# Performance work log

Hardware: AMD Instinct MI355X
Metric: run time of the kernel (lower is better)

The kernel has to match this reference:

```python
import jax, jax.numpy as jnp
import numpy as np
from itertools import product

SPATIAL1 = (41, 1600, 1408)  # (z,y,x) = grid[::-1] + [1,0,0]
NUM_BATCH = 2
BN_EPS = 1e-3

# ---------- numpy rulebook construction (spconv-style, done once on host) ----------

def _encode(c, shape):
    D, H, W = [int(v) for v in shape]
    return ((c[:, 0].astype(np.int64) * D + c[:, 1]) * H + c[:, 2]) * W + c[:, 3]

def _lookup(skeys, order, cand):
    pos = np.clip(np.searchsorted(skeys, cand), 0, len(skeys) - 1)
    hit = skeys[pos] == cand
    return hit, order[pos]

def _pad_rb(pairs, n_in, n_out):
    P = max(max(len(a) for a, _ in pairs), 1)
    K = len(pairs)
    ii = np.full((K, P), n_in, np.int32)   # sentinel -> zero feature row
    oo = np.full((K, P), n_out, np.int32)  # sentinel -> dummy output row
    for k, (a, b) in enumerate(pairs):
        ii[k, :len(a)] = a
        oo[k, :len(b)] = b
    return ii, oo

def _subm_rb(coords, shape):
    # SubMConv3d k=3 p=1 s=1: output sites == input sites
    N = len(coords)
    keys = _encode(coords, shape)
    order = np.argsort(keys); skeys = keys[order]
    dims = np.array(shape)
    pairs = []
    for off in product((-1, 0, 1), repeat=3):
        nb = coords[:, 1:] + np.array(off)
        ok = (nb >= 0).all(1) & (nb < dims).all(1)
        oid = np.nonzero(ok)[0]
        cand = _encode(np.concatenate([coords[ok, :1], nb[ok]], 1), shape)
        hit, iid = _lookup(skeys, order, cand)
        pairs.append((iid[hit].astype(np.int32), oid[hit].astype(np.int32)))
    return _pad_rb(pairs, N, N)

def _down_rb(coords, in_shape, ks, st, pd):
    # SparseConv3d: output site active iff any kernel tap hits an active input
    dims = np.array(in_shape); ks = np.array(ks); st = np.array(st); pd = np.array(pd)
    out_shape = (dims + 2 * pd - ks) // st + 1
    offs = list(product(*[range(int(k)) for k in ks]))
    outs = []
    for off in offs:
        o = coords[:, 1:] + pd - np.array(off)
        ok = (o % st == 0).all(1)
        od = o // st
        ok &= (od >= 0).all(1) & (od < out_shape).all(1)
        outs.append(np.concatenate([coords[ok, :1], od[ok]], 1))
    out_coords = np.unique(np.concatenate(outs, 0), axis=0)
    keys = _encode(coords, in_shape)
    order = np.argsort(keys); skeys = keys[order]
    pairs = []
    for off in offs:
        ic = out_coords[:, 1:] * st - pd + np.array(off)
        ok = (ic >= 0).all(1) & (ic < dims).all(1)
        oid = np.nonzero(ok)[0]
        cand = _encode(np.concatenate([out_coords[ok, :1], ic[ok]], 1), in_shape)
        hit, iid = _lookup(skeys, order, cand)
        pairs.append((iid[hit].astype(np.int32), oid[hit].astype(np.int32)))
    ii, oo = _pad_rb(pairs, len(coords), len(out_coords))
    return ii, oo, out_coords, tuple(int(v) for v in out_shape)

def _gen_coords(rng):
    # clustered LiDAR-like active voxels (surfaces -> local density)
    D, H, W = SPATIAL1
    per = []
    for b in range(NUM_BATCH):
        centers = rng.integers([3, 30, 30], [D - 4, H - 31, W - 31], size=(600, 3))
        pts = centers[:, None, :] + rng.integers(-3, 4, size=(600, 60, 3))
        pts = np.clip(pts.reshape(-1, 3), 0, np.array([D - 1, H - 1, W - 1]))
        uniq = np.unique(pts, axis=0)
        per.append(np.concatenate([np.full((len(uniq), 1), b, np.int64), uniq], 1))
    return np.concatenate(per, 0)

CHANS = [(27, 4, 16), (27, 16, 16), (27, 16, 32), (27, 32, 32), (27, 32, 32),
         (27, 32, 64), (27, 64, 64), (27, 64, 64), (27, 64, 64), (27, 64, 64),
         (27, 64, 64), (3, 64, 128)]

def setup_inputs() -> dict:
    rng = np.random.default_rng(0)
    coords = _gen_coords(rng)  # (N,4) [b,z,y,x]
    N = len(coords)
    s1i, s1o = _subm_rb(coords, SPATIAL1)
    d2i, d2o, c2, s2 = _down_rb(coords, SPATIAL1, (3, 3, 3), (2, 2, 2), (1, 1, 1))
    s2i, s2o = _subm_rb(c2, s2)
    d3i, d3o, c3, s3 = _down_rb(c2, s2, (3, 3, 3), (2, 2, 2), (1, 1, 1))
    s3i, s3o = _subm_rb(c3, s3)
    d4i, d4o, c4, s4 = _down_rb(c3, s3, (3, 3, 3), (2, 2, 2), (0, 1, 1))
    s4i, s4o = _subm_rb(c4, s4)
    oi, oo, c5, s5 = _down_rb(c4, s4, (3, 1, 1), (2, 1, 1), (0, 0, 0))

    key = jax.random.key(0)
    ks = jax.random.split(key, 40)
    inp = {}
    for i, (K, ci, co) in enumerate(CHANS):
        inp[f"w{i}"] = (jax.random.normal(ks[i], (K, ci, co), jnp.float32)
                         / np.sqrt(K * ci)).astype(jnp.float32)
        kb = jax.random.split(ks[12 + i], 4)
        inp[f"bn{i}"] = jnp.stack([
            jax.random.uniform(kb[0], (co,)) + 0.5,   # gamma
            jax.random.normal(kb[1], (co,)) * 0.1,    # beta
            jax.random.normal(kb[2], (co,)) * 0.1,    # running mean
            jax.random.uniform(kb[3], (co,)) + 0.5,   # running var
        ]).astype(jnp.float32)
    inp["voxels"] = jax.random.normal(ks[30], (N, 5, 4), jnp.float32)
    inp["voxel_num_points"] = jax.random.randint(ks[31], (N,), 0, 6).astype(jnp.int32)
    for name, arr in [("subm1_in", s1i), ("subm1_out", s1o), ("down2_in", d2i),
                      ("down2_out", d2o), ("subm2_in", s2i), ("subm2_out", s2o),
                      ("down3_in", d3i), ("down3_out", d3o), ("subm3_in", s3i),
                      ("subm3_out", s3o), ("down4_in", d4i), ("down4_out", d4o),
                      ("subm4_in", s4i), ("subm4_out", s4o), ("out_in", oi),
                      ("out_out", oo)]:
        inp[name] = jnp.asarray(arr)
    inp["batch_idx"] = jnp.asarray(c5[:, 0].astype(np.int32))
    inp["n2"] = len(c2); inp["n3"] = len(c3); inp["n4"] = len(c4); inp["n5"] = len(c5)
    inp["n_batch"] = NUM_BATCH
    return inp

# ---------- jax forward ----------

def _sconv(feats, w, in_idx, out_idx, n_out):
    # gather -> per-kernel-offset GEMM -> scatter-add (spconv implicit GEMM)
    fpad = jnp.concatenate([feats, jnp.zeros((1, feats.shape[1]), feats.dtype)], 0)
    g = fpad[in_idx]                                  # (K,P,Cin)
    contrib = jnp.einsum('kpi,kio->kpo', g, w)        # (K,P,Cout)
    out = jnp.zeros((n_out + 1, w.shape[2]), feats.dtype)
    return out.at[out_idx].add(contrib)[:n_out]

def _bnrelu(x, bn):
    g, b, m, v = bn  # eval-mode BatchNorm1d, eps=1e-3
    return jax.nn.relu((x - m) * jax.lax.rsqrt(v + BN_EPS) * g + b)

def reference(voxels, voxel_num_points, w0, w1, w2, w3, w4, w5, w6, w7, w8, w9,
              w10, w11, bn0, bn1, bn2, bn3, bn4, bn5, bn6, bn7, bn8, bn9, bn10,
              bn11, subm1_in, subm1_out, down2_in, down2_out, subm2_in, subm2_out,
              down3_in, down3_out, subm3_in, subm3_out, down4_in, down4_out,
              subm4_in, subm4_out, out_in, out_out, batch_idx, n2, n3, n4, n5,
              n_batch):
    # mean-VFE: average point features per voxel
    denom = jnp.maximum(voxel_num_points.astype(voxels.dtype), 1.0)[:, None]
    x = voxels.sum(1) / denom                              # (N,4)
    n1 = x.shape[0]
    x = _bnrelu(_sconv(x, w0, subm1_in, subm1_out, n1), bn0)   # conv_input
    x = _bnrelu(_sconv(x, w1, subm1_in, subm1_out, n1), bn1)   # conv1
    x = _bnrelu(_sconv(x, w2, down2_in, down2_out, n2), bn2)   # conv2 (s2)
    x = _bnrelu(_sconv(x, w3, subm2_in, subm2_out, n2), bn3)
    x = _bnrelu(_sconv(x, w4, subm2_in, subm2_out, n2), bn4)
    x = _bnrelu(_sconv(x, w5, down3_in, down3_out, n3), bn5)   # conv3 (s2)
    x = _bnrelu(_sconv(x, w6, subm3_in, subm3_out, n3), bn6)
    x = _bnrelu(_sconv(x, w7, subm3_in, subm3_out, n3), bn7)
    x = _bnrelu(_sconv(x, w8, down4_in, down4_out, n4), bn8)   # conv4 (s2)
    x = _bnrelu(_sconv(x, w9, subm4_in, subm4_out, n4), bn9)
    x = _bnrelu(_sconv(x, w10, subm4_in, subm4_out, n4), bn10)
    x = _bnrelu(_sconv(x, w11, out_in, out_out, n5), bn11)     # conv_out
    # dc_feats: per-sample global max pool over active voxels (== max_pool1d)
    dc = jax.ops.segment_max(x, batch_idx, num_segments=n_batch)
    return dc
```

## Files before the change

### kernel.cpp

```cpp
#include <hip/hip_runtime.h>

#define TPB 256
typedef unsigned short u16;
typedef __attribute__((ext_vector_type(8))) short short8v;
typedef __attribute__((ext_vector_type(4))) float f32x4;

__device__ __forceinline__ u16 f2bf(float x) {
    unsigned u = __float_as_uint(x);
    return (u16)((u + 0x7FFFu + ((u >> 16) & 1u)) >> 16);
}
__device__ __forceinline__ float bf2f(u16 h) {
    return __uint_as_float(((unsigned)h) << 16);
}

template<int CS>
__device__ __forceinline__ int swzc(int r, int c) {
    constexpr int PH = (CS == 8) ? 0 : 1;
    return c ^ ((r >> PH) & (CS - 1));
}

__device__ __forceinline__ int xcd_swz(int bid, int nwg) {
    int q = nwg >> 3, r = nwg & 7;
    int x = bid & 7, idx = bid >> 3;
    return (x < r ? x * (q + 1) : r * (q + 1) + (x - r) * q) + idx;
}

__device__ __forceinline__ void gld16(const u16* g, u16* l) {
    __builtin_amdgcn_global_load_lds(
        (const __attribute__((address_space(1))) void*)g,
        (__attribute__((address_space(3))) void*)l, 16, 0, 0);
}

__global__ void vfe_kernel(const float* __restrict__ voxels,
                           const int* __restrict__ nump,
                           float* __restrict__ x, int N) {
    int i = blockIdx.x * blockDim.x + threadIdx.x;
    if (i >= N * 4) return;
    int n = i >> 2, c = i & 3;
    const float* v = voxels + (long)n * 20 + c;
    float s = v[0] + v[4] + v[8] + v[12] + v[16];
    x[i] = s / fmaxf((float)nump[n], 1.0f);
}

struct IBE { const int* rin; const int* rout; int* inv; int P, K, n_in, n_out, KP; };
struct IBA { IBE e[8]; };
__global__ void inv_build_all_kernel(IBA a, long grand) {
    long t = (long)blockIdx.x * blockDim.x + threadIdx.x;
    if (t >= grand) return;
    #pragma unroll
    for (int i = 0; i < 8; ++i) {
        if (t < a.e[i].KP) {
            const IBE& E = a.e[i];
            int ii = E.rin[t];
            if (ii != E.n_in) {
                int k = (int)(t / E.P);
                E.inv[(long)k * E.n_out + E.rout[t]] = ii;
            }
            return;
        }
        t -= a.e[i].KP;
    }
}

struct WPE { const float* w; u16* oh; u16* ol; int K, ci, co, total, paired; };
struct WPA { WPE e[11]; };
__global__ void wprep_kernel(WPA a, long grand) {
    long t = (long)blockIdx.x * blockDim.x + threadIdx.x;
    if (t >= grand) return;
    #pragma unroll
    for (int i = 0; i < 11; ++i) {
        if (t < a.e[i].total) {
            const WPE& E = a.e[i];
            if (E.paired) {
                int p = (int)(t / (E.co * 32));
                int rem = (int)(t % (E.co * 32));
                int o = rem / 32, ci = rem % 32;
                int tap = 2 * p + (ci >> 4);
                float x = (tap < 27) ? E.w[((long)tap * 16 + (ci & 15)) * E.co + o] : 0.f;
                u16 h = f2bf(x);
                float lf = x - bf2f(h);
                int ch = ci >> 3, e = ci & 7;
                int sch = ch ^ ((o >> 1) & 3);
                long d = ((long)p * E.co + o) * 32 + sch * 8 + e;
                E.oh[d] = h; E.ol[d] = f2bf(lf);
            } else {
                int cc = E.ci * E.co;
                int k = (int)(t / cc), r = (int)(t % cc), c = r / E.co, o = r % E.co;
                float x = E.w[t];
                u16 h = f2bf(x);
                float lf = x - bf2f(h);
                int cs = E.ci >> 3, ph = (cs == 8) ? 0 : 1;
                int ch = c >> 3, e = c & 7;
                int sch = ch ^ ((o >> ph) & (cs - 1));
                long d = ((long)k * E.co + o) * E.ci + sch * 8 + e;
                E.oh[d] = h; E.ol[d] = f2bf(lf);
            }
            return;
        }
        t -= a.e[i].total;
    }
}

template<int CO, int K>
__global__ __launch_bounds__(256)
void dconv4_kernel(const float* __restrict__ feats,
                   const float* __restrict__ w,
                   const float* __restrict__ bn,
                   const int* __restrict__ inv, int inv_n,
                   u16* __restrict__ oh, u16* __restrict__ ol,
                   int n_out) {
    constexpr int OG = CO / 4;
    __shared__ float sW[K * 4 * CO];
    for (int i = threadIdx.x; i < K * 4 * CO; i += 256) sW[i] = w[i];
    __syncthreads();
    long t = (long)blockIdx.x * 256 + threadIdx.x;
    int row = (int)(t / OG), og = (int)(t % OG);
    if (row >= n_out) return;
    float a0 = 0.f, a1 = 0.f, a2 = 0.f, a3 = 0.f;
    for (int k = 0; k < K; ++k) {
        int idx = inv[(long)k * inv_n + row];
        if (idx < 0) continue;
        float4 av = *(const float4*)(feats + (long)idx * 4);
        const float* wk = sW + k * 4 * CO + og * 4;
        #pragma unroll
        for (int ci = 0; ci < 4; ++ci) {
            float a = (&av.x)[ci];
            a0 = fmaf(a, wk[ci * CO + 0], a0);
            a1 = fmaf(a, wk[ci * CO + 1], a1);
            a2 = fmaf(a, wk[ci * CO + 2], a2);
            a3 = fmaf(a, wk[ci * CO + 3], a3);
        }
    }
    float4 g = *(const float4*)(bn + og * 4);
    float4 b = *(const float4*)(bn + CO + og * 4);
    float4 m = *(const float4*)(bn + 2 * CO + og * 4);
    float4 v = *(const float4*)(bn + 3 * CO + og * 4);
    float o4[4];
    o4[0] = fmaxf((a0 - m.x) * rsqrtf(v.x + 1e-3f) * g.x + b.x, 0.f);
    o4[1] = fmaxf((a1 - m.y) * rsqrtf(v.y + 1e-3f) * g.y + b.y, 0.f);
    o4[2] = fmaxf((a2 - m.z) * rsqrtf(v.z + 1e-3f) * g.z + b.z, 0.f);
    o4[3] = fmaxf((a3 - m.w) * rsqrtf(v.w + 1e-3f) * g.w + b.w, 0.f);
    long base = (long)row * CO + og * 4;
    #pragma unroll
    for (int c = 0; c < 4; ++c) {
        u16 h = f2bf(o4[c]);
        oh[base + c] = h;
        ol[base + c] = f2bf(o4[c] - bf2f(h));
    }
}

template<int CI, int CO, int KPt, int KT, bool PAIRED, int EPI>
__global__ __launch_bounds__(256, 4)
void mconv_kernel(const u16* __restrict__ fh, const u16* __restrict__ fl,
                  const u16* __restrict__ wh, const u16* __restrict__ wl,
                  const int* __restrict__ inv,
                  const u16* __restrict__ zpage,
                  float* __restrict__ part, long slab_elems,
                  const float* __restrict__ bn,
                  u16* __restrict__ oh, u16* __restrict__ ol,
                  float* __restrict__ outf,
                  int n_out, int kpb) {
    constexpr int CS  = CI / 8;
    constexpr int LCS = (CS == 8) ? 3 : 2;
    constexpr int PH  = (CS == 8) ? 0 : 1;
    constexpr int KS  = CI / 32;
    constexpr int WC  = (CO >= 32) ? 2 : 1;
    constexpr int MT  = (WC == 2) ? 2 : 1;
    constexpr int NTW = CO / (16 * WC);
    constexpr int ASL = 64 * CS;
    constexpr int BSL = CO * CS;
    constexpr int AIT = (ASL + 255) / 256;
    constexpr int BIT = (BSL + 255) / 256;

    __shared__ __align__(16) u16 sAh[64 * CI];
    __shared__ __align__(16) u16 sAl[64 * CI];
    __shared__ __align__(16) u16 sBh[CO * CI];
    __shared__ __align__(16) u16 sBl[CO * CI];

    const int t = threadIdx.x;
    const int bx = xcd_swz(blockIdx.x, gridDim.x);
    const int brow = bx * 64;
    const int kbeg = blockIdx.y * kpb;
    const int kend = (kbeg + kpb < KPt) ? (kbeg + kpb) : KPt;

    const int lane = t & 63, wid = t >> 6;
    const int wr = wid / WC, wc = wid % WC;
    const int frow = lane & 15;
    const int fch  = lane >> 4;

    f32x4 acc[MT][NTW];
    #pragma unroll
    for (int mt = 0; mt < MT; ++mt)
        #pragma unroll
        for (int nt = 0; nt < NTW; ++nt) {
            acc[mt][nt][0] = 0.f; acc[mt][nt][1] = 0.f;
            acc[mt][nt][2] = 0.f; acc[mt][nt][3] = 0.f;
        }

    auto stage = [&](int k) {
        #pragma unroll
        for (int s = 0; s < AIT; ++s) {
            int slot = s * 256 + t;
            if (ASL % 256 == 0 || slot < ASL) {
                int r = slot >> LCS, cc = slot & (CS - 1);
                int c = cc ^ ((r >> PH) & (CS - 1));
                int grow = brow + r;
                const u16 *srcH, *srcL;
                if (PAIRED) {
                    int tap = 2 * k + (c >> 1);
                    int idx = (grow < n_out && tap < KT)
                              ? inv[(long)tap * n_out + grow] : -1;
                    srcH = (idx >= 0) ? fh + (long)idx * 16 + (c & 1) * 8 : zpage;
                    srcL = (idx >= 0) ? fl + (long)idx * 16 + (c & 1) * 8 : zpage;
                } else {
                    int idx = (grow < n_out) ? inv[(long)k * n_out + grow] : -1;
                    srcH = (idx >= 0) ? fh + (long)idx * CI + c * 8 : zpage;
                    srcL = (idx >= 0) ? fl + (long)idx * CI + c * 8 : zpage;
                }
                gld16(srcH, sAh + (s * 256 + wid * 64) * 8);
                gld16(srcL, sAl + (s * 256 + wid * 64) * 8);
            }
        }
        const u16* gbh = wh + (long)k * CO * CI;
        const u16* gbl = wl + (long)k * CO * CI;
        #pragma unroll
        for (int s = 0; s < BIT; ++s) {
            int slot = s * 256 + t;
            if (BSL % 256 == 0 || slot < BSL) {
                gld16(gbh + (long)slot * 8, sBh + (s * 256 + wid * 64) * 8);
                gld16(gbl + (long)slot * 8, sBl + (s * 256 + wid * 64) * 8);
            }
        }
    };
    auto compute = [&]() {
        #pragma unroll
        for (int ks = 0; ks < KS; ++ks) {
            int c = ks * 4 + fch;
            short8v ah[MT], al[MT];
            #pragma unroll
            for (int mt = 0; mt < MT; ++mt) {
                int r = wr * (MT * 16) + mt * 16 + frow;
                int o = r * CI + swzc<CS>(r, c) * 8;
                ah[mt] = *(const short8v*)(sAh + o);
                al[mt] = *(const short8v*)(sAl + o);
            }
            #pragma unroll
            for (int nt = 0; nt < NTW; ++nt) {
                int col = wc * (CO / WC) + nt * 16 + frow;
                int o = col * CI + swzc<CS>(col, c) * 8;
                short8v bh = *(const short8v*)(sBh + o);
                short8v bl = *(const short8v*)(sBl + o);
                #pragma unroll
                for (int mt = 0; mt < MT; ++mt) {
                    acc[mt][nt] = __builtin_amdgcn_mfma_f32_16x16x32_bf16(ah[mt], bh, acc[mt][nt], 0, 0, 0);
                    acc[mt][nt] = __builtin_amdgcn_mfma_f32_16x16x32_bf16(ah[mt], bl, acc[mt][nt], 0, 0, 0);
                    acc[mt][nt] = __builtin_amdgcn_mfma_f32_16x16x32_bf16(al[mt], bh, acc[mt][nt], 0, 0, 0);
                }
            }
        }
    };

    for (int k = kbeg; k < kend; ++k) {
        stage(k);
        __syncthreads();
        compute();
        if (k + 1 < kend) __syncthreads();
    }

    if constexpr (EPI == 0) {
        float* dst = part + (long)blockIdx.y * slab_elems;
        #pragma unroll
        for (int mt = 0; mt < MT; ++mt) {
            int orow0 = brow + wr * (MT * 16) + mt * 16 + (lane >> 4) * 4;
            #pragma unroll
            for (int nt = 0; nt < NTW; ++nt) {
                int ocol = wc * (CO / WC) + nt * 16 + (lane & 15);
                #pragma unroll
                for (int j = 0; j < 4; ++j) {
                    int r = orow0 + j;
                    if (r < n_out) dst[(long)r * CO + ocol] = acc[mt][nt][j];
                }
            }
        }
    } else {
        #pragma unroll
        for (int mt = 0; mt < MT; ++mt) {
            int orow0 = brow + wr * (MT * 16) + mt * 16 + (lane >> 4) * 4;
            #pragma unroll
            for (int nt = 0; nt < NTW; ++nt) {
                int ocol = wc * (CO / WC) + nt * 16 + (lane & 15);
                float g = bn[ocol], bb = bn[CO + ocol];
                float m = bn[2 * CO + ocol], vv = bn[3 * CO + ocol];
                float sc = rsqrtf(vv + 1e-3f) * g;
                #pragma unroll
                for (int j = 0; j < 4; ++j) {
                    int r = orow0 + j;
                    if (r < n_out) {
                        float yv = fmaxf((acc[mt][nt][j] - m) * sc + bb, 0.f);
                        if constexpr (EPI == 1) {
                            u16 h = f2bf(yv);
                            oh[(long)r * CO + ocol] = h;
                            ol[(long)r * CO + ocol] = f2bf(yv - bf2f(h));
                        } else {
                            outf[(long)r * CO + ocol] = yv;
                        }
                    }
                }
            }
        }
    }
}

template<bool EMIT16>
__global__ void reduce_bnrelu_kernel(const float* __restrict__ part, long stride,
                                     int ys, const float* __restrict__ bn, int co,
                                     float* __restrict__ outf,
                                     u16* __restrict__ oh, u16* __restrict__ ol,
                                     long total) {
    long t = (long)blockIdx.x * blockDim.x + threadIdx.x;
    if (t >= total) return;
    float s = 0.f;
    for (int y = 0; y < ys; ++y) s += part[(long)y * stride + t];
    int o = (int)(t % co);
    float g = bn[o], b = bn[co + o], m = bn[2 * co + o], v = bn[3 * co + o];
    float yv = fmaxf((s - m) * rsqrtf(v + 1e-3f) * g + b, 0.f);
    if (EMIT16) {
        u16 h = f2bf(yv);
        oh[t] = h;
        ol[t] = f2bf(yv - bf2f(h));
    } else {
        outf[t] = yv;
    }
}

__global__ void segmax_kernel(const float* __restrict__ x,
                              const int* __restrict__ bidx,
                              float* __restrict__ out, int rows, int nb) {
    __shared__ float sM[8 * 128];
    for (int i = threadIdx.x; i < nb * 128; i += 256) sM[i] = 0.f;
    __syncthreads();
    int c = threadIdx.x & 127;
    int sub = threadIdx.x >> 7;
    for (int r = blockIdx.x * 2 + sub; r < rows; r += gridDim.x * 2) {
        float v = x[(long)r * 128 + c];
        int b = bidx[r];
        atomicMax((int*)&sM[b * 128 + c], __float_as_int(v));
    }
    __syncthreads();
    for (int i = threadIdx.x; i < nb * 128; i += 256)
        atomicMax((int*)out + i, __float_as_int(sM[i]));
}

extern "C" void kernel_launch(void* const* d_in, const int* in_sizes, int n_in,
                              void* d_out, int out_size, void* d_ws, size_t ws_size,
                              hipStream_t stream) {
    (void)n_in;
    const float* voxels = (const float*)d_in[24];
    const int*   nump   = (const int*)d_in[25];
    const int N  = in_sizes[25];
    const int n2 = in_sizes[30] / 27;
    const int n3 = in_sizes[34] / 27;
    const int n4 = in_sizes[38] / 27;
    const int n5 = in_sizes[42];

    struct L { int wi, rb, K, ci, co, nin, nout; };
    const L layers[12] = {
        {0,  26, 27,  4,  16, N,  N }, {1,  26, 27, 16,  16, N,  N },
        {2,  28, 27, 16,  32, N,  n2}, {3,  30, 27, 32,  32, n2, n2},
        {4,  30, 27, 32,  32, n2, n2}, {5,  32, 27, 32,  64, n2, n3},
        {6,  34, 27, 64,  64, n3, n3}, {7,  34, 27, 64,  64, n3, n3},
        {8,  36, 27, 64,  64, n3, n4}, {9,  38, 27, 64,  64, n4, n4},
        {10, 38, 27, 64,  64, n4, n4}, {11, 40,  3, 64, 128, n4, n5},
    };
    struct RBD { int rb, K, nin, nout; };
    const RBD rbs[8] = {
        {26, 27, N,  N }, {28, 27, N,  n2}, {30, 27, n2, n2}, {32, 27, n2, n3},
        {34, 27, n3, n3}, {36, 27, n3, n4}, {38, 27, n4, n4}, {40, 3,  n4, n5},
    };
    const int invmap[12] = {0, 0, 1, 2, 2, 3, 4, 4, 5, 6, 6, 7};

    size_t feat_elems = (size_t)N * 4, wt_elems = 0, arena_elems = 0;
    for (int i = 0; i < 12; ++i) {
        size_t fe = (size_t)layers[i].nout * layers[i].co;
        if (fe > feat_elems) feat_elems = fe;
        if (i >= 3) wt_elems += (size_t)layers[i].K * layers[i].ci * layers[i].co;
    }
    for (int r = 0; r < 8; ++r) arena_elems += (size_t)rbs[r].nout * rbs[r].K;
    const size_t wp1_elems = 14 * 32 * 16;
    const size_t wp2_elems = 14 * 32 * 32;
    auto al = [](size_t x) { return (x + 255) & ~(size_t)255; };
    char* p = (char*)d_ws;
    u16*   zpage = (u16*)p; p += 256;
    int*   inv_arena = (int*)p; p += al(arena_elems * 4);
    float* bufA = (float*)p; p += al(feat_elems * 4);
    u16* ph[2]; u16* pl[2];
    ph[0] = (u16*)p; p += al(feat_elems * 2);
    pl[0] = (u16*)p; p += al(feat_elems * 2);
    ph[1] = (u16*)p; p += al(feat_elems * 2);
    pl[1] = (u16*)p; p += al(feat_elems * 2);
    u16* wth = (u16*)p; p += al(wt_elems * 2);
    u16* wtl = (u16*)p; p += al(wt_elems * 2);
    u16* wp1h = (u16*)p; p += al(wp1_elems * 2);
    u16* wp1l = (u16*)p; p += al(wp1_elems * 2);
    u16* wp2h = (u16*)p; p += al(wp2_elems * 2);
    u16* wp2l = (u16*)p; p += al(wp2_elems * 2);
    float* slab = (float*)p;
    size_t slab_budget = ws_size - (size_t)((char*)slab - (char*)d_ws);

    hipMemsetAsync(zpage, 0, 256, stream);

    int* invs[8];
    {
        size_t off = 0;
        for (int r = 0; r < 8; ++r) { invs[r] = inv_arena + off; off += (size_t)rbs[r].nout * rbs[r].K; }
        hipMemsetAsync(inv_arena, 0xFF, arena_elems * sizeof(int), stream);
        IBA ia;
        long grand = 0;
        for (int r = 0; r < 8; ++r) {
            int P  = in_sizes[rbs[r].rb] / rbs[r].K;
            ia.e[r].rin  = (const int*)d_in[rbs[r].rb];
            ia.e[r].rout = (const int*)d_in[rbs[r].rb + 1];
            ia.e[r].inv  = invs[r];
            ia.e[r].P = P; ia.e[r].K = rbs[r].K; ia.e[r].n_in = rbs[r].nin;
            ia.e[r].n_out = rbs[r].nout;
            ia.e[r].KP = rbs[r].K * P;
            grand += ia.e[r].KP;
        }
        inv_build_all_kernel<<<dim3((unsigned)((grand + TPB - 1) / TPB)), dim3(TPB), 0, stream>>>(ia, grand);
    }

    {
        long tot = (long)N * 4;
        vfe_kernel<<<dim3((unsigned)((tot + TPB - 1) / TPB)), dim3(TPB), 0, stream>>>(
            voxels, nump, bufA, N);
    }

    size_t woff[9];
    {
        WPA wa;
        size_t off = 0;
        for (int i = 0; i < 9; ++i) {
            const L& l = layers[i + 3];
            woff[i] = off;
            wa.e[i].w  = (const float*)d_in[2 * l.wi];
            wa.e[i].oh = wth + off;
            wa.e[i].ol = wtl + off;
            wa.e[i].K = l.K; wa.e[i].ci = l.ci; wa.e[i].co = l.co;
            wa.e[i].total = l.K * l.ci * l.co;
            wa.e[i].paired = 0;
            off += (size_t)wa.e[i].total;
        }
        wa.e[9]  = { (const float*)d_in[2], wp1h, wp1l, 27, 16, 16, (int)wp1_elems, 1 };
        wa.e[10] = { (const float*)d_in[4], wp2h, wp2l, 27, 16, 32, (int)wp2_elems, 1 };
        long grand = (long)off + wp1_elems + wp2_elems;
        wprep_kernel<<<dim3((unsigned)((grand + TPB - 1) / TPB)), dim3(TPB), 0, stream>>>(wa, grand);
    }

    {
        const L& l = layers[0];
        long tot = (long)l.nout * 4;
        dconv4_kernel<16, 27><<<dim3((unsigned)((tot + 255) / 256)), 256, 0, stream>>>(
            bufA, (const float*)d_in[0], (const float*)d_in[1], invs[0], l.nout,
            ph[0], pl[0], l.nout);
    }

    int cset = 0;
    for (int i = 1; i < 12; ++i) {
        const L& l = layers[i];
        const int* invp = invs[invmap[i]];
        unsigned blocks = (unsigned)((l.nout + 63) / 64);
        int KPv = (i <= 2) ? 14 : l.K;
        int ysmax = (KPv == 14) ? 9 : ((KPv == 27) ? 27 : 3);
        size_t per = (size_t)l.nout * l.co * 4;
        int ys = 1;
        while (ys < ysmax && blocks * (unsigned)ys < 768) ys *= 3;
        if (ys > ysmax) ys = ysmax;
        while (ys > 1 && (size_t)ys * per > slab_budget) ys /= 3;
        int kpb = (KPv + ys - 1) / ys;
        long slab_elems = (long)l.nout * l.co;
        dim3 grid(blocks, (unsigned)ys);
        const float* bn = (const float*)d_in[2 * l.wi + 1];
        const u16* fh = ph[cset];
        const u16* fl = pl[cset];
        const u16* whp = (i >= 3) ? wth + woff[i - 3] : nullptr;
        const u16* wlp = (i >= 3) ? wtl + woff[i - 3] : nullptr;

        #define MCONV(CI_, CO_, KP_, KT_, PRD_, WH_, WL_)                              \
            do {                                                                       \
                if (ys == 1 && i < 11)                                                 \
                    mconv_kernel<CI_, CO_, KP_, KT_, PRD_, 1><<<grid, 256, 0, stream>>>( \
                        fh, fl, WH_, WL_, invp, zpage, nullptr, 0, bn,                 \
                        ph[cset ^ 1], pl[cset ^ 1], nullptr, l.nout, kpb);             \
                else if (ys == 1)                                                      \
                    mconv_kernel<CI_, CO_, KP_, KT_, PRD_, 2><<<grid, 256, 0, stream>>>( \
                        fh, fl, WH_, WL_, invp, zpage, nullptr, 0, bn,                 \
                        nullptr, nullptr, bufA, l.nout, kpb);                          \
                else                                                                   \
                    mconv_kernel<CI_, CO_, KP_, KT_, PRD_, 0><<<grid, 256, 0, stream>>>( \
                        fh, fl, WH_, WL_, invp, zpage, slab, slab_elems, bn,           \
                        nullptr, nullptr, nullptr, l.nout, kpb);                       \
            } while (0)

        switch (i) {
        case 1:          MCONV(32, 16, 14, 27, true,  wp1h, wp1l); break;
        case 2:          MCONV(32, 32, 14, 27, true,  wp2h, wp2l); break;
        case 3: case 4:  MCONV(32, 32, 27, 27, false, whp, wlp);   break;
        case 5:          MCONV(32, 64, 27, 27, false, whp, wlp);   break;
        case 11:         MCONV(64, 128, 3, 3,  false, whp, wlp);   break;
        default:         MCONV(64, 64, 27, 27, false, whp, wlp);   break;
        }
        #undef MCONV

        if (ys == 1) {
            if (i < 11) cset ^= 1;
        } else {
            long total = (long)l.nout * l.co;
            unsigned rblocks = (unsigned)((total + TPB - 1) / TPB);
            if (i < 11) {
                reduce_bnrelu_kernel<true><<<dim3(rblocks), dim3(TPB), 0, stream>>>(
                    slab, slab_elems, ys, bn, l.co,
                    nullptr, ph[cset ^ 1], pl[cset ^ 1], total);
                cset ^= 1;
            } else {
                reduce_bnrelu_kernel<false><<<dim3(rblocks), dim3(TPB), 0, stream>>>(
                    slab, slab_elems, ys, bn, l.co, bufA, nullptr, nullptr, total);
            }
        }
    }

    hipMemsetAsync(d_out, 0, (size_t)out_size * sizeof(float), stream);
    const int* bidx = (const int*)d_in[42];
    int nb = out_size / 128;
    segmax_kernel<<<dim3(128), dim3(256), 0, stream>>>(bufA, bidx, (float*)d_out, n5, nb);
}
```

Before: 406.4 us.

## Pair kernel taps for 32-channel subm layers and vectorize reduce-BN kernel

Extends the tap-pairing scheme, which packs two kernel taps into one K-step, from the 16-channel-input layers to layers 3 and 4 (32-channel input, CI=64 tile). Those layers now run 14 K-steps instead of 27, aiming for better MFMA K utilization and fewer synchronisation rounds. The weight-prep kernel is generalised to build paired layouts for any per-tap channel count. The split-K reduce+BN+ReLU kernel now handles four elements per thread with float4/ushort4 accesses. The trade-offs are a doubled A/B shared-memory footprint for the paired layers and a zero-padded 28th tap.

```diff
diff --git a/kernel.cpp b/kernel.cpp
--- a/kernel.cpp
+++ b/kernel.cpp
@@ -62,7 +62,7 @@
     }
 }
 
-struct WPE { const float* w; u16* oh; u16* ol; int K, ci, co, total, paired; };
+struct WPE { const float* w; u16* oh; u16* ol; int K, ci, co, total, pci; };
 struct WPA { WPE e[11]; };
 __global__ void wprep_kernel(WPA a, long grand) {
     long t = (long)blockIdx.x * blockDim.x + threadIdx.x;
@@ -71,17 +71,20 @@
     for (int i = 0; i < 11; ++i) {
         if (t < a.e[i].total) {
             const WPE& E = a.e[i];
-            if (E.paired) {
-                int p = (int)(t / (E.co * 32));
-                int rem = (int)(t % (E.co * 32));
-                int o = rem / 32, ci = rem % 32;
-                int tap = 2 * p + (ci >> 4);
-                float x = (tap < 27) ? E.w[((long)tap * 16 + (ci & 15)) * E.co + o] : 0.f;
+            if (E.pci) {
+                int ci2 = 2 * E.pci;
+                int p = (int)(t / (E.co * ci2));
+                int rem = (int)(t % (E.co * ci2));
+                int o = rem / ci2, ci = rem % ci2;
+                int tap = 2 * p + ci / E.pci;
+                float x = (tap < 27)
+                    ? E.w[((long)tap * E.pci + (ci % E.pci)) * E.co + o] : 0.f;
                 u16 h = f2bf(x);
                 float lf = x - bf2f(h);
+                int cs = ci2 >> 3, ph = (cs == 8) ? 0 : 1;
                 int ch = ci >> 3, e = ci & 7;
-                int sch = ch ^ ((o >> 1) & 3);
-                long d = ((long)p * E.co + o) * 32 + sch * 8 + e;
+                int sch = ch ^ ((o >> ph) & (cs - 1));
+                long d = ((long)p * E.co + o) * ci2 + sch * 8 + e;
                 E.oh[d] = h; E.ol[d] = f2bf(lf);
             } else {
                 int cc = E.ci * E.co;
@@ -149,7 +152,7 @@
     }
 }
 
-template<int CI, int CO, int KPt, int KT, bool PAIRED, int EPI>
+template<int CI, int CO, int KPt, int KT, bool PAIRED, int PCI, int EPI>
 __global__ __launch_bounds__(256, 4)
 void mconv_kernel(const u16* __restrict__ fh, const u16* __restrict__ fl,
                   const u16* __restrict__ wh, const u16* __restrict__ wl,
@@ -171,6 +174,7 @@
     constexpr int BSL = CO * CS;
     constexpr int AIT = (ASL + 255) / 256;
     constexpr int BIT = (BSL + 255) / 256;
+    constexpr int SUBCS = PAIRED ? (PCI / 8) : 1;
 
     __shared__ __align__(16) u16 sAh[64 * CI];
     __shared__ __align__(16) u16 sAl[64 * CI];
@@ -207,11 +211,12 @@
                 int grow = brow + r;
                 const u16 *srcH, *srcL;
                 if (PAIRED) {
-                    int tap = 2 * k + (c >> 1);
+                    int tap = 2 * k + c / SUBCS;
+                    int within = c % SUBCS;
                     int idx = (grow < n_out && tap < KT)
                               ? inv[(long)tap * n_out + grow] : -1;
-                    srcH = (idx >= 0) ? fh + (long)idx * 16 + (c & 1) * 8 : zpage;
-                    srcL = (idx >= 0) ? fl + (long)idx * 16 + (c & 1) * 8 : zpage;
+                    srcH = (idx >= 0) ? fh + (long)idx * PCI + within * 8 : zpage;
+                    srcL = (idx >= 0) ? fl + (long)idx * PCI + within * 8 : zpage;
                 } else {
                     int idx = (grow < n_out) ? inv[(long)k * n_out + grow] : -1;
                     srcH = (idx >= 0) ? fh + (long)idx * CI + c * 8 : zpage;
@@ -316,20 +321,33 @@
                                      int ys, const float* __restrict__ bn, int co,
                                      float* __restrict__ outf,
                                      u16* __restrict__ oh, u16* __restrict__ ol,
-                                     long total) {
-    long t = (long)blockIdx.x * blockDim.x + threadIdx.x;
-    if (t >= total) return;
-    float s = 0.f;
-    for (int y = 0; y < ys; ++y) s += part[(long)y * stride + t];
-    int o = (int)(t % co);
-    float g = bn[o], b = bn[co + o], m = bn[2 * co + o], v = bn[3 * co + o];
-    float yv = fmaxf((s - m) * rsqrtf(v + 1e-3f) * g + b, 0.f);
+                                     long total4) {
+    long t4 = (long)blockIdx.x * blockDim.x + threadIdx.x;
+    if (t4 >= total4) return;
+    long base = t4 * 4;
+    float4 s = make_float4(0.f, 0.f, 0.f, 0.f);
+    for (int y = 0; y < ys; ++y) {
+        float4 v = *(const float4*)(part + (long)y * stride + base);
+        s.x += v.x; s.y += v.y; s.z += v.z; s.w += v.w;
+    }
+    int o = (int)(base % co);
+    float4 g = *(const float4*)(bn + o);
+    float4 b = *(const float4*)(bn + co + o);
+    float4 m = *(const float4*)(bn + 2 * co + o);
+    float4 v = *(const float4*)(bn + 3 * co + o);
+    float y0 = fmaxf((s.x - m.x) * rsqrtf(v.x + 1e-3f) * g.x + b.x, 0.f);
+    float y1 = fmaxf((s.y - m.y) * rsqrtf(v.y + 1e-3f) * g.y + b.y, 0.f);
+    float y2 = fmaxf((s.z - m.z) * rsqrtf(v.z + 1e-3f) * g.z + b.z, 0.f);
+    float y3 = fmaxf((s.w - m.w) * rsqrtf(v.w + 1e-3f) * g.w + b.w, 0.f);
     if (EMIT16) {
-        u16 h = f2bf(yv);
-        oh[t] = h;
-        ol[t] = f2bf(yv - bf2f(h));
+        u16 h0 = f2bf(y0), h1 = f2bf(y1), h2 = f2bf(y2), h3 = f2bf(y3);
+        ushort4 hv = { h0, h1, h2, h3 };
+        ushort4 lv = { f2bf(y0 - bf2f(h0)), f2bf(y1 - bf2f(h1)),
+                       f2bf(y2 - bf2f(h2)), f2bf(y3 - bf2f(h3)) };
+        *(ushort4*)(oh + base) = hv;
+        *(ushort4*)(ol + base) = lv;
     } else {
-        outf[t] = yv;
+        *(float4*)(outf + base) = make_float4(y0, y1, y2, y3);
     }
 }
 
@@ -379,15 +397,22 @@
     };
     const int invmap[12] = {0, 0, 1, 2, 2, 3, 4, 4, 5, 6, 6, 7};
 
-    size_t feat_elems = (size_t)N * 4, wt_elems = 0, arena_elems = 0;
+    size_t feat_elems = (size_t)N * 4, wst_elems = 0, arena_elems = 0;
+    size_t wst_off[12];
     for (int i = 0; i < 12; ++i) {
         size_t fe = (size_t)layers[i].nout * layers[i].co;
         if (fe > feat_elems) feat_elems = fe;
-        if (i >= 3) wt_elems += (size_t)layers[i].K * layers[i].ci * layers[i].co;
+        if (i >= 5) { wst_off[i] = wst_elems;
+                      wst_elems += (size_t)layers[i].K * layers[i].ci * layers[i].co; }
     }
     for (int r = 0; r < 8; ++r) arena_elems += (size_t)rbs[r].nout * rbs[r].K;
-    const size_t wp1_elems = 14 * 32 * 16;
-    const size_t wp2_elems = 14 * 32 * 32;
+    const int pair_pci[4] = {16, 16, 32, 32};
+    const int pair_co[4]  = {16, 32, 32, 32};
+    size_t wpd_elems[4], wpd_off[4], wpd_tot = 0;
+    for (int j = 0; j < 4; ++j) {
+        wpd_elems[j] = (size_t)14 * pair_co[j] * 2 * pair_pci[j];
+        wpd_off[j] = wpd_tot; wpd_tot += wpd_elems[j];
+    }
     auto al = [](size_t x) { return (x + 255) & ~(size_t)255; };
     char* p = (char*)d_ws;
     u16*   zpage = (u16*)p; p += 256;
@@ -398,12 +423,10 @@
     pl[0] = (u16*)p; p += al(feat_elems * 2);
     ph[1] = (u16*)p; p += al(feat_elems * 2);
     pl[1] = (u16*)p; p += al(feat_elems * 2);
-    u16* wth = (u16*)p; p += al(wt_elems * 2);
-    u16* wtl = (u16*)p; p += al(wt_elems * 2);
-    u16* wp1h = (u16*)p; p += al(wp1_elems * 2);
-    u16* wp1l = (u16*)p; p += al(wp1_elems * 2);
-    u16* wp2h = (u16*)p; p += al(wp2_elems * 2);
-    u16* wp2l = (u16*)p; p += al(wp2_elems * 2);
+    u16* wth = (u16*)p; p += al(wst_elems * 2);
+    u16* wtl = (u16*)p; p += al(wst_elems * 2);
+    u16* wph = (u16*)p; p += al(wpd_tot * 2);
+    u16* wpl = (u16*)p; p += al(wpd_tot * 2);
     float* slab = (float*)p;
     size_t slab_budget = ws_size - (size_t)((char*)slab - (char*)d_ws);
 
@@ -435,24 +458,30 @@
             voxels, nump, bufA, N);
     }
 
-    size_t woff[9];
     {
         WPA wa;
-        size_t off = 0;
-        for (int i = 0; i < 9; ++i) {
-            const L& l = layers[i + 3];
-            woff[i] = off;
-            wa.e[i].w  = (const float*)d_in[2 * l.wi];
-            wa.e[i].oh = wth + off;
-            wa.e[i].ol = wtl + off;
-            wa.e[i].K = l.K; wa.e[i].ci = l.ci; wa.e[i].co = l.co;
-            wa.e[i].total = l.K * l.ci * l.co;
-            wa.e[i].paired = 0;
-            off += (size_t)wa.e[i].total;
-        }
-        wa.e[9]  = { (const float*)d_in[2], wp1h, wp1l, 27, 16, 16, (int)wp1_elems, 1 };
-        wa.e[10] = { (const float*)d_in[4], wp2h, wp2l, 27, 16, 32, (int)wp2_elems, 1 };
-        long grand = (long)off + wp1_elems + wp2_elems;
+        long grand = 0;
+        for (int i = 5; i < 12; ++i) {
+            const L& l = layers[i];
+            WPE& E = wa.e[i - 5];
+            E.w  = (const float*)d_in[2 * l.wi];
+            E.oh = wth + wst_off[i];
+            E.ol = wtl + wst_off[i];
+            E.K = l.K; E.ci = l.ci; E.co = l.co;
+            E.total = l.K * l.ci * l.co;
+            E.pci = 0;
+            grand += E.total;
+        }
+        for (int j = 0; j < 4; ++j) {
+            WPE& E = wa.e[7 + j];
+            E.w  = (const float*)d_in[2 * layers[1 + j].wi];
+            E.oh = wph + wpd_off[j];
+            E.ol = wpl + wpd_off[j];
+            E.K = 27; E.ci = pair_pci[j]; E.co = pair_co[j];
+            E.total = (int)wpd_elems[j];
+            E.pci = pair_pci[j];
+            grand += E.total;
+        }
         wprep_kernel<<<dim3((unsigned)((grand + TPB - 1) / TPB)), dim3(TPB), 0, stream>>>(wa, grand);
     }
 
@@ -469,7 +498,7 @@
         const L& l = layers[i];
         const int* invp = invs[invmap[i]];
         unsigned blocks = (unsigned)((l.nout + 63) / 64);
-        int KPv = (i <= 2) ? 14 : l.K;
+        int KPv = (i <= 4) ? 14 : l.K;
         int ysmax = (KPv == 14) ? 9 : ((KPv == 27) ? 27 : 3);
         size_t per = (size_t)l.nout * l.co * 4;
         int ys = 1;
@@ -482,48 +511,48 @@
         const float* bn = (const float*)d_in[2 * l.wi + 1];
         const u16* fh = ph[cset];
         const u16* fl = pl[cset];
-        const u16* whp = (i >= 3) ? wth + woff[i - 3] : nullptr;
-        const u16* wlp = (i >= 3) ? wtl + woff[i - 3] : nullptr;
-
-        #define MCONV(CI_, CO_, KP_, KT_, PRD_, WH_, WL_)                              \
+        const u16* whp = (i >= 5) ? wth + wst_off[i] : wph + wpd_off[i - 1];
+        const u16* wlp = (i >= 5) ? wtl + wst_off[i] : wpl + wpd_off[i - 1];
+
+        #define MCONV(CI_, CO_, KP_, KT_, PRD_, PCI_)                                  \
             do {                                                                       \
                 if (ys == 1 && i < 11)                                                 \
-                    mconv_kernel<CI_, CO_, KP_, KT_, PRD_, 1><<<grid, 256, 0, stream>>>( \
-                        fh, fl, WH_, WL_, invp, zpage, nullptr, 0, bn,                 \
+                    mconv_kernel<CI_, CO_, KP_, KT_, PRD_, PCI_, 1><<<grid, 256, 0, stream>>>( \
+                        fh, fl, whp, wlp, invp, zpage, nullptr, 0, bn,                 \
                         ph[cset ^ 1], pl[cset ^ 1], nullptr, l.nout, kpb);             \
                 else if (ys == 1)                                                      \
-                    mconv_kernel<CI_, CO_, KP_, KT_, PRD_, 2><<<grid, 256, 0, stream>>>( \
-                        fh, fl, WH_, WL_, invp, zpage, nullptr, 0, bn,                 \
+                    mconv_kernel<CI_, CO_, KP_, KT_, PRD_, PCI_, 2><<<grid, 256, 0, stream>>>( \
+                        fh, fl, whp, wlp, invp, zpage, nullptr, 0, bn,                 \
                         nullptr, nullptr, bufA, l.nout, kpb);                          \
                 else                                                                   \
-                    mconv_kernel<CI_, CO_, KP_, KT_, PRD_, 0><<<grid, 256, 0, stream>>>( \
-                        fh, fl, WH_, WL_, invp, zpage, slab, slab_elems, bn,           \
+                    mconv_kernel<CI_, CO_, KP_, KT_, PRD_, PCI_, 0><<<grid, 256, 0, stream>>>( \
+                        fh, fl, whp, wlp, invp, zpage, slab, slab_elems, bn,           \
                         nullptr, nullptr, nullptr, l.nout, kpb);                       \
             } while (0)
 
         switch (i) {
-        case 1:          MCONV(32, 16, 14, 27, true,  wp1h, wp1l); break;
-        case 2:          MCONV(32, 32, 14, 27, true,  wp2h, wp2l); break;
-        case 3: case 4:  MCONV(32, 32, 27, 27, false, whp, wlp);   break;
-        case 5:          MCONV(32, 64, 27, 27, false, whp, wlp);   break;
-        case 11:         MCONV(64, 128, 3, 3,  false, whp, wlp);   break;
-        default:         MCONV(64, 64, 27, 27, false, whp, wlp);   break;
+        case 1:          MCONV(32, 16, 14, 27, true, 16);  break;
+        case 2:          MCONV(32, 32, 14, 27, true, 16);  break;
+        case 3: case 4:  MCONV(64, 32, 14, 27, true, 32);  break;
+        case 5:          MCONV(32, 64, 27, 27, false, 32); break;
+        case 11:         MCONV(64, 128, 3, 3, false, 64);  break;
+        default:         MCONV(64, 64, 27, 27, false, 64); break;
         }
         #undef MCONV
 
         if (ys == 1) {
             if (i < 11) cset ^= 1;
         } else {
-            long total = (long)l.nout * l.co;
-            unsigned rblocks = (unsigned)((total + TPB - 1) / TPB);
+            long total4 = ((long)l.nout * l.co) / 4;
+            unsigned rblocks = (unsigned)((total4 + TPB - 1) / TPB);
             if (i < 11) {
                 reduce_bnrelu_kernel<true><<<dim3(rblocks), dim3(TPB), 0, stream>>>(
                     slab, slab_elems, ys, bn, l.co,
-                    nullptr, ph[cset ^ 1], pl[cset ^ 1], total);
+                    nullptr, ph[cset ^ 1], pl[cset ^ 1], total4);
                 cset ^= 1;
             } else {
                 reduce_bnrelu_kernel<false><<<dim3(rblocks), dim3(TPB), 0, stream>>>(
-                    slab, slab_elems, ys, bn, l.co, bufA, nullptr, nullptr, total);
+                    slab, slab_elems, ys, bn, l.co, bufA, nullptr, nullptr, total4);
             }
         }
     }
```

Result: faster. 390.0 us (-4.0%).
